# Kernel tuning notes

Measured on AMD Instinct MI355X. Metric: run time of the kernel, lower is better.

## Reference

```python
import jax, jax.numpy as jnp
import numpy as np

HEADS = 8
WSZ = 8
DIM_KEY = 32
DIM_VALUE = 32
DIM = 256
EPS = 1e-5


def setup_inputs() -> dict:
    key = jax.random.key(0)
    ks = jax.random.split(key, 8)
    B, C, H, W = 16, DIM, 128, 128
    inner_k = DIM_KEY * HEADS
    inner_v = DIM_VALUE * HEADS
    x = jax.random.normal(ks[0], (B, C, H, W), dtype=jnp.float32)
    g = jnp.ones((C,), dtype=jnp.float32)
    b = jnp.zeros((C,), dtype=jnp.float32)
    wq = jax.random.normal(ks[1], (inner_k, C), dtype=jnp.float32) * (C ** -0.5)
    wk = jax.random.normal(ks[2], (inner_k, C), dtype=jnp.float32) * (C ** -0.5)
    wv = jax.random.normal(ks[3], (inner_v, C), dtype=jnp.float32) * (C ** -0.5)
    local_w = jax.random.normal(ks[4], (inner_v, inner_v, 3, 3), dtype=jnp.float32) * ((inner_v * 9) ** -0.5)
    local_b = jnp.zeros((inner_v,), dtype=jnp.float32)
    out_w = jax.random.normal(ks[5], (C, inner_v), dtype=jnp.float32) * (inner_v ** -0.5)
    out_b = jnp.zeros((C,), dtype=jnp.float32)
    return {"x": x, "g": g, "b": b, "wq": wq, "wk": wk, "wv": wv,
            "local_w": local_w, "local_b": local_b, "out_w": out_w, "out_b": out_b}


def _to_windows(t, heads, wsz):
    # [B, heads*d, H, W] -> [B*X*Y, heads, wsz*wsz, d]
    B, Ch, H, W = t.shape
    d = Ch // heads
    X, Y = H // wsz, W // wsz
    t = t.reshape(B, heads, d, X, wsz, Y, wsz)
    t = t.transpose(0, 3, 5, 1, 4, 6, 2)  # B X Y heads w1 w2 d
    return t.reshape(B * X * Y, heads, wsz * wsz, d)


def _from_windows(t, B, heads, wsz, H, W):
    X, Y = H // wsz, W // wsz
    d = t.shape[-1]
    t = t.reshape(B, X, Y, heads, wsz, wsz, d)
    t = t.transpose(0, 3, 6, 1, 4, 2, 5)  # B heads d X w1 Y w2
    return t.reshape(B, heads * d, H, W)


def reference(x, g, b, wq, wk, wv, local_w, local_b, out_w, out_b):
    B, C, H, W = x.shape
    # ChanLayerNorm over channel dim (biased var)
    mean = jnp.mean(x, axis=1, keepdims=True)
    var = jnp.var(x, axis=1, keepdims=True)
    xn = (x - mean) / jnp.sqrt(var + EPS) * g[None, :, None, None] + b[None, :, None, None]
    # 1x1 conv projections as einsum
    q = jnp.einsum('oc,bchw->bohw', wq, xn)
    k = jnp.einsum('oc,bchw->bohw', wk, xn)
    v = jnp.einsum('oc,bchw->bohw', wv, xn)
    # local interactive 3x3 conv on v
    local_out = jax.lax.conv_general_dilated(
        v, local_w, window_strides=(1, 1), padding='SAME',
        dimension_numbers=('NCHW', 'OIHW', 'NCHW')) + local_b[None, :, None, None]
    # windowed attention
    qw = _to_windows(q, HEADS, WSZ)
    kw = _to_windows(k, HEADS, WSZ)
    vw = _to_windows(v, HEADS, WSZ)
    scale = DIM_KEY ** -0.5
    dots = jnp.einsum('whid,whjd->whij', qw, kw) * scale
    attn = jax.nn.softmax(dots, axis=-1)
    out = jnp.einsum('whij,whjd->whid', attn, vw)
    out = _from_windows(out, B, HEADS, WSZ, H, W)
    out = out + local_out
    # to_out 1x1 conv with bias
    return jnp.einsum('oc,bchw->bohw', out_w, out) + out_b[None, :, None, None]
```

## Files before the change

### kernel.cpp

```cpp
#include <hip/hip_runtime.h>

typedef __attribute__((ext_vector_type(8))) short short8;
typedef __attribute__((ext_vector_type(4))) float f32x4;
typedef __attribute__((ext_vector_type(2))) _Float16 h2;

#define DEV static __device__ __forceinline__

typedef __attribute__((address_space(1))) void GVoid;
typedef __attribute__((address_space(3))) void LVoid;

DEV unsigned short f2bf(float f) {
  unsigned u = __builtin_bit_cast(unsigned, f);
  u += 0x7fffu + ((u >> 16) & 1u);
  return (unsigned short)(u >> 16);
}
DEV float bf2f(unsigned short h) {
  unsigned u = ((unsigned)h) << 16;
  return __builtin_bit_cast(float, u);
}
DEV void cp16(void* lds_uniform_base, const void* gsrc) {
  __builtin_amdgcn_global_load_lds((GVoid*)gsrc, (LVoid*)lds_uniform_base, 16, 0, 0);
}
DEV float fdot2(h2 a, h2 b, float c) {
  return __builtin_amdgcn_fdot2(a, b, c, false);
}
DEV h2 bch2(float f) { return __builtin_bit_cast(h2, f); }

DEV void xcd_remap(int& mb, int& nb) {
  const int gx = gridDim.x;
  const int p = blockIdx.x + gx * blockIdx.y;
  const int nwg = gx * gridDim.y;
  const int q = nwg >> 3;
  const int L = (p & 7) * q + (p >> 3);
  mb = L % gx;
  nb = L / gx;
}

__global__ __launch_bounds__(256) void setup_kernel(
    const float* __restrict__ wq, const float* __restrict__ wk, const float* __restrict__ wv,
    const float* __restrict__ lw, const float* __restrict__ ow,
    unsigned short* __restrict__ wqkvb, unsigned short* __restrict__ w2b,
    unsigned short* __restrict__ woutb, unsigned short* __restrict__ zp)
{
  int i = blockIdx.x * 256 + threadIdx.x;
  if (i < 196608) {
    float f = (i < 65536) ? wq[i] : (i < 131072) ? wk[i - 65536] : wv[i - 131072];
    wqkvb[i] = f2bf(f);
  } else if (i < 786432) {
    int j = i - 196608;
    int co = j / 2304;
    int r = j - co * 2304;
    int tap = r >> 8;
    int ci = r & 255;
    w2b[j] = f2bf(lw[(co * 256 + ci) * 9 + tap]);
  } else if (i < 851968) {
    int j = i - 786432;
    woutb[j] = f2bf(ow[j]);
  } else if (i < 852096) {
    zp[i - 851968] = 0;
  }
}

__global__ __launch_bounds__(256) void ln_kernel(
    const float* __restrict__ x, const float* __restrict__ gw,
    const float* __restrict__ bw, unsigned short* __restrict__ xn)
{
  const int t = threadIdx.x;
  const int p = blockIdx.x * 256 + t;
  const int b = p >> 14;
  const int pix = p & 16383;
  const int h = pix >> 7;
  const int w = pix & 127;
  const float* xp = x + ((size_t)b << 22) + pix;

  float sum = 0.f, ss = 0.f;
#pragma unroll 8
  for (int c = 0; c < 256; ++c) {
    float f = xp[(size_t)c << 14];
    sum += f;
    ss += f * f;
  }
  float mean = sum * (1.f / 256.f);
  float var = ss * (1.f / 256.f) - mean * mean;
  float inv = rsqrtf(var + 1e-5f);

  const int pw = ((b * 16 + (h >> 3)) * 16 + (w >> 3)) * 64 + (h & 7) * 8 + (w & 7);
  unsigned short* op = xn + (size_t)pw * 256;
#pragma unroll 2
  for (int c = 0; c < 256; c += 4) {
    float f0 = xp[(size_t)(c + 0) << 14];
    float f1 = xp[(size_t)(c + 1) << 14];
    float f2 = xp[(size_t)(c + 2) << 14];
    float f3 = xp[(size_t)(c + 3) << 14];
    float v0 = (f0 - mean) * inv * gw[c + 0] + bw[c + 0];
    float v1 = (f1 - mean) * inv * gw[c + 1] + bw[c + 1];
    float v2 = (f2 - mean) * inv * gw[c + 2] + bw[c + 2];
    float v3 = (f3 - mean) * inv * gw[c + 3] + bw[c + 3];
    unsigned long long pk = (unsigned long long)f2bf(v0) |
                            ((unsigned long long)f2bf(v1) << 16) |
                            ((unsigned long long)f2bf(v2) << 32) |
                            ((unsigned long long)f2bf(v3) << 48);
    *(unsigned long long*)(op + c) = pk;
  }
}

DEV void mfma_tile(const unsigned short* As, const unsigned short* Bs,
                   int wm, int wn, int l15, int quad, f32x4 (&acc)[4][4])
{
  const int sx = l15 & 7;
#pragma unroll
  for (int ks = 0; ks < 2; ++ks) {
    const int sl = ((ks * 4 + quad) ^ sx) * 8;
    short8 a[4], b[4];
#pragma unroll
    for (int i = 0; i < 4; ++i)
      a[i] = *(const short8*)(As + (wm + i * 16 + l15) * 64 + sl);
#pragma unroll
    for (int j = 0; j < 4; ++j)
      b[j] = *(const short8*)(Bs + (wn + j * 16 + l15) * 64 + sl);
#pragma unroll
    for (int i = 0; i < 4; ++i)
#pragma unroll
      for (int j = 0; j < 4; ++j)
        acc[i][j] = __builtin_amdgcn_mfma_f32_16x16x32_bf16(a[i], b[j], acc[i][j], 0, 0, 0);
  }
}

__global__ __launch_bounds__(256) void qkv_gemm(
    const unsigned short* __restrict__ wqkvb, const unsigned short* __restrict__ xn,
    unsigned short* __restrict__ qb, unsigned short* __restrict__ kb,
    unsigned short* __restrict__ vb)
{
  __shared__ __align__(16) unsigned short As[128 * 64];
  __shared__ __align__(16) unsigned short Bs[128 * 64];
  const int tid = threadIdx.x;
  const int lane = tid & 63;
  const int wave = tid >> 6;
  const int l15 = lane & 15;
  const int quad = lane >> 4;
  const int wm = (wave >> 1) * 64;
  const int wn = (wave & 1) * 64;
  const int sub = tid & 7;
  const int row0 = tid >> 3;
  const int ssub = sub ^ (row0 & 7);
  int mb, nb;
  xcd_remap(mb, nb);
  const int m0 = mb * 128;
  const int n0 = nb * 128;

  f32x4 acc[4][4];
  f32x4 zero = {0.f, 0.f, 0.f, 0.f};
#pragma unroll
  for (int i = 0; i < 4; ++i)
#pragma unroll
    for (int j = 0; j < 4; ++j) acc[i][j] = zero;

  for (int kt = 0; kt < 4; ++kt) {
    const int k0 = kt * 64;
#pragma unroll
    for (int it = 0; it < 4; ++it) {
      const int row = it * 32 + row0;
      cp16(As + (size_t)(it * 256 + wave * 64) * 8,
           wqkvb + (size_t)(m0 + row) * 256 + k0 + ssub * 8);
      cp16(Bs + (size_t)(it * 256 + wave * 64) * 8,
           xn + (size_t)(n0 + row) * 256 + k0 + ssub * 8);
    }
    __syncthreads();
    mfma_tile(As, Bs, wm, wn, l15, quad, acc);
    __syncthreads();
  }

  unsigned short* ob = (m0 < 256) ? qb : (m0 < 512) ? kb : vb;
  const int chb = (m0 & 255) + wm;
#pragma unroll
  for (int i = 0; i < 4; ++i) {
    const int ch = chb + i * 16 + quad * 4;
#pragma unroll
    for (int j = 0; j < 4; ++j) {
      const int n = n0 + wn + j * 16 + l15;
      unsigned long long pk = (unsigned long long)f2bf(acc[i][j][0]) |
                              ((unsigned long long)f2bf(acc[i][j][1]) << 16) |
                              ((unsigned long long)f2bf(acc[i][j][2]) << 32) |
                              ((unsigned long long)f2bf(acc[i][j][3]) << 48);
      *(unsigned long long*)(ob + (size_t)n * 256 + ch) = pk;
    }
  }
}

__global__ __launch_bounds__(128) void attn_kernel(
    const unsigned short* __restrict__ qb, const unsigned short* __restrict__ kb,
    const unsigned short* __restrict__ vb, unsigned short* __restrict__ attnb)
{
  __shared__ __align__(16) _Float16 ks2[2][64][40];
  __shared__ __align__(16) _Float16 vs2[2][32][64];
  const int tid = threadIdx.x;
  const int tok = tid & 63;
  const int hs = tid >> 6;
  const int win = blockIdx.x >> 2;
  const int head = (blockIdx.x & 3) * 2 + hs;
  const size_t base = (size_t)(win * 64 + tok) * 256 + head * 32;

  h2 q2[16];
  {
    const uint4* qp4 = (const uint4*)(qb + base);
    const uint4* kp4 = (const uint4*)(kb + base);
    const uint4* vp4 = (const uint4*)(vb + base);
#pragma unroll
    for (int i = 0; i < 4; ++i) {
      uint4 u = qp4[i];
      unsigned uu[4] = {u.x, u.y, u.z, u.w};
#pragma unroll
      for (int w = 0; w < 4; ++w) {
        h2 p;
        p.x = (_Float16)bf2f((unsigned short)(uu[w] & 0xffff));
        p.y = (_Float16)bf2f((unsigned short)(uu[w] >> 16));
        q2[i * 4 + w] = p;
      }
    }
#pragma unroll
    for (int i = 0; i < 4; ++i) {
      uint4 u = kp4[i];
      unsigned uu[4] = {u.x, u.y, u.z, u.w};
#pragma unroll
      for (int w = 0; w < 4; ++w) {
        int c = 2 * (i * 4 + w);
        ks2[hs][tok][c + 0] = (_Float16)bf2f((unsigned short)(uu[w] & 0xffff));
        ks2[hs][tok][c + 1] = (_Float16)bf2f((unsigned short)(uu[w] >> 16));
      }
      uint4 v = vp4[i];
      unsigned vv[4] = {v.x, v.y, v.z, v.w};
#pragma unroll
      for (int w = 0; w < 4; ++w) {
        int c = 2 * (i * 4 + w);
        vs2[hs][c + 0][tok] = (_Float16)bf2f((unsigned short)(vv[w] & 0xffff));
        vs2[hs][c + 1][tok] = (_Float16)bf2f((unsigned short)(vv[w] >> 16));
      }
    }
  }
  __syncthreads();

  float dots[64];
#pragma unroll 4
  for (int j = 0; j < 64; ++j) {
    const float4* kr = (const float4*)ks2[hs][j];
    float d = 0.f;
#pragma unroll
    for (int qq = 0; qq < 4; ++qq) {
      float4 raw = kr[qq];
      d = fdot2(q2[4 * qq + 0], bch2(raw.x), d);
      d = fdot2(q2[4 * qq + 1], bch2(raw.y), d);
      d = fdot2(q2[4 * qq + 2], bch2(raw.z), d);
      d = fdot2(q2[4 * qq + 3], bch2(raw.w), d);
    }
    dots[j] = d * 0.17677669529663688f;
  }
  float mx = -1e30f;
#pragma unroll
  for (int j = 0; j < 64; ++j) mx = fmaxf(mx, dots[j]);
  float s = 0.f;
#pragma unroll
  for (int j = 0; j < 64; ++j) {
    float e = __expf(dots[j] - mx);
    dots[j] = e;
    s += e;
  }
  const float rs = 1.f / s;

  h2 p2[32];
#pragma unroll
  for (int jp = 0; jp < 32; ++jp) {
    h2 p;
    p.x = (_Float16)dots[2 * jp];
    p.y = (_Float16)dots[2 * jp + 1];
    p2[jp] = p;
  }

  float of[32];
#pragma unroll 4
  for (int c = 0; c < 32; ++c) {
    const float4* vr = (const float4*)vs2[hs][c];
    float o = 0.f;
#pragma unroll
    for (int qq = 0; qq < 8; ++qq) {
      float4 raw = vr[qq];
      o = fdot2(p2[4 * qq + 0], bch2(raw.x), o);
      o = fdot2(p2[4 * qq + 1], bch2(raw.y), o);
      o = fdot2(p2[4 * qq + 2], bch2(raw.z), o);
      o = fdot2(p2[4 * qq + 3], bch2(raw.w), o);
    }
    of[c] = o;
  }

  uint4* op4 = (uint4*)(attnb + base);
#pragma unroll
  for (int i = 0; i < 4; ++i) {
    uint4 o;
    o.x = (unsigned)f2bf(of[8 * i + 0] * rs) | ((unsigned)f2bf(of[8 * i + 1] * rs) << 16);
    o.y = (unsigned)f2bf(of[8 * i + 2] * rs) | ((unsigned)f2bf(of[8 * i + 3] * rs) << 16);
    o.z = (unsigned)f2bf(of[8 * i + 4] * rs) | ((unsigned)f2bf(of[8 * i + 5] * rs) << 16);
    o.w = (unsigned)f2bf(of[8 * i + 6] * rs) | ((unsigned)f2bf(of[8 * i + 7] * rs) << 16);
    op4[i] = o;
  }
}

__global__ __launch_bounds__(256) void conv_gemm(
    const unsigned short* __restrict__ w2b, const unsigned short* __restrict__ vbuf,
    const unsigned short* __restrict__ attnb, const float* __restrict__ lbias,
    const unsigned short* __restrict__ zp, unsigned short* __restrict__ sumb)
{
  __shared__ __align__(16) unsigned short As[128 * 64];
  __shared__ __align__(16) unsigned short Bs[128 * 64];
  const int tid = threadIdx.x;
  const int lane = tid & 63;
  const int wave = tid >> 6;
  const int l15 = lane & 15;
  const int quad = lane >> 4;
  const int wm = (wave >> 1) * 64;
  const int wn = (wave & 1) * 64;
  const int sub = tid & 7;
  const int row0 = tid >> 3;
  const int ssub = sub ^ (row0 & 7);
  int mb, nb;
  xcd_remap(mb, nb);
  const int m0 = mb * 128;
  const int n0 = nb * 128;

  int bi[4], hh[4], ww[4];
#pragma unroll
  for (int it = 0; it < 4; ++it) {
    int n = n0 + it * 32 + row0;
    int b = n >> 14;
    int r = n & 16383;
    int Xw = r >> 10;
    int r2 = r & 1023;
    int Yw = r2 >> 6;
    int t2 = r2 & 63;
    bi[it] = b;
    hh[it] = Xw * 8 + (t2 >> 3);
    ww[it] = Yw * 8 + (t2 & 7);
  }

  f32x4 acc[4][4];
  f32x4 zero = {0.f, 0.f, 0.f, 0.f};
#pragma unroll
  for (int i = 0; i < 4; ++i)
#pragma unroll
    for (int j = 0; j < 4; ++j) acc[i][j] = zero;

  for (int tap = 0; tap < 9; ++tap) {
    const int dy = tap / 3 - 1;
    const int dx = tap - (tap / 3) * 3 - 1;
    const unsigned short* bp[4];
    int bstep[4];
#pragma unroll
    for (int it = 0; it < 4; ++it) {
      int h2_ = hh[it] + dy, w2_ = ww[it] + dx;
      bool ok = ((unsigned)h2_ < 128u) && ((unsigned)w2_ < 128u);
      int nn = ((bi[it] * 16 + (h2_ >> 3)) * 16 + (w2_ >> 3)) * 64 + (h2_ & 7) * 8 + (w2_ & 7);
      bp[it] = ok ? (vbuf + (size_t)nn * 256 + ssub * 8) : (zp + ssub * 8);
      bstep[it] = ok ? 64 : 0;
    }
    for (int cc = 0; cc < 4; ++cc) {
#pragma unroll
      for (int it = 0; it < 4; ++it) {
        cp16(As + (size_t)(it * 256 + wave * 64) * 8,
             w2b + ((size_t)(m0 + it * 32 + row0) * 9 + tap) * 256 + cc * 64 + ssub * 8);
        cp16(Bs + (size_t)(it * 256 + wave * 64) * 8, bp[it] + cc * bstep[it]);
      }
      __syncthreads();
      mfma_tile(As, Bs, wm, wn, l15, quad, acc);
      __syncthreads();
    }
  }

#pragma unroll
  for (int i = 0; i < 4; ++i) {
    const int ch = m0 + wm + i * 16 + quad * 4;
    const float b0 = lbias[ch + 0], b1 = lbias[ch + 1], b2 = lbias[ch + 2], b3 = lbias[ch + 3];
#pragma unroll
    for (int j = 0; j < 4; ++j) {
      const int n = n0 + wn + j * 16 + l15;
      const unsigned* ap = (const unsigned*)(attnb + (size_t)n * 256 + ch);
      unsigned a0 = ap[0], a1 = ap[1];
      float r0 = acc[i][j][0] + b0 + bf2f((unsigned short)(a0 & 0xffff));
      float r1 = acc[i][j][1] + b1 + bf2f((unsigned short)(a0 >> 16));
      float r2 = acc[i][j][2] + b2 + bf2f((unsigned short)(a1 & 0xffff));
      float r3 = acc[i][j][3] + b3 + bf2f((unsigned short)(a1 >> 16));
      unsigned long long pk = (unsigned long long)f2bf(r0) |
                              ((unsigned long long)f2bf(r1) << 16) |
                              ((unsigned long long)f2bf(r2) << 32) |
                              ((unsigned long long)f2bf(r3) << 48);
      *(unsigned long long*)(sumb + (size_t)n * 256 + ch) = pk;
    }
  }
}

__global__ __launch_bounds__(256) void out_gemm(
    const unsigned short* __restrict__ woutb, const unsigned short* __restrict__ sumb,
    const float* __restrict__ obias, float* __restrict__ out)
{
  __shared__ __align__(16) unsigned short As[128 * 64];
  __shared__ __align__(16) unsigned short Bs[128 * 64];
  const int tid = threadIdx.x;
  const int lane = tid & 63;
  const int wave = tid >> 6;
  const int l15 = lane & 15;
  const int quad = lane >> 4;
  const int wm = (wave >> 1) * 64;
  const int wn = (wave & 1) * 64;
  const int sub = tid & 7;
  const int row0 = tid >> 3;
  const int ssub = sub ^ (row0 & 7);
  int mb, nb;
  xcd_remap(mb, nb);
  const int m0 = mb * 128;
  const int n0 = nb * 128;

  f32x4 acc[4][4];
  f32x4 zero = {0.f, 0.f, 0.f, 0.f};
#pragma unroll
  for (int i = 0; i < 4; ++i)
#pragma unroll
    for (int j = 0; j < 4; ++j) acc[i][j] = zero;

  for (int kt = 0; kt < 4; ++kt) {
    const int k0 = kt * 64;
#pragma unroll
    for (int it = 0; it < 4; ++it) {
      const int row = it * 32 + row0;
      cp16(As + (size_t)(it * 256 + wave * 64) * 8,
           woutb + (size_t)(m0 + row) * 256 + k0 + ssub * 8);
      cp16(Bs + (size_t)(it * 256 + wave * 64) * 8,
           sumb + (size_t)(n0 + row) * 256 + k0 + ssub * 8);
    }
    __syncthreads();
    mfma_tile(As, Bs, wm, wn, l15, quad, acc);
    __syncthreads();
  }

  int bb4[4], hw4[4];
#pragma unroll
  for (int j = 0; j < 4; ++j) {
    int n = n0 + wn + j * 16 + l15;
    int b = n >> 14;
    int r = n & 16383;
    int Xw = r >> 10;
    int r2 = r & 1023;
    int Yw = r2 >> 6;
    int t2 = r2 & 63;
    bb4[j] = b;
    hw4[j] = (Xw * 8 + (t2 >> 3)) * 128 + Yw * 8 + (t2 & 7);
  }
#pragma unroll
  for (int i = 0; i < 4; ++i) {
    const int mb2 = m0 + wm + i * 16 + quad * 4;
    const float o0 = obias[mb2 + 0], o1 = obias[mb2 + 1], o2 = obias[mb2 + 2], o3 = obias[mb2 + 3];
#pragma unroll
    for (int j = 0; j < 4; ++j) {
      float* o = out + ((size_t)(bb4[j] * 256 + mb2) << 14) + hw4[j];
      o[0] = acc[i][j][0] + o0;
      o[(size_t)1 << 14] = acc[i][j][1] + o1;
      o[(size_t)2 << 14] = acc[i][j][2] + o2;
      o[(size_t)3 << 14] = acc[i][j][3] + o3;
    }
  }
}

extern "C" void kernel_launch(void* const* d_in, const int* in_sizes, int n_in,
                              void* d_out, int out_size, void* d_ws, size_t ws_size,
                              hipStream_t stream)
{
  const float* x  = (const float*)d_in[0];
  const float* g  = (const float*)d_in[1];
  const float* bb = (const float*)d_in[2];
  const float* wq = (const float*)d_in[3];
  const float* wk = (const float*)d_in[4];
  const float* wv = (const float*)d_in[5];
  const float* lw = (const float*)d_in[6];
  const float* lb = (const float*)d_in[7];
  const float* ow = (const float*)d_in[8];
  const float* ob = (const float*)d_in[9];
  float* out = (float*)d_out;

  char* ws = (char*)d_ws;
  unsigned short* wqkvb = (unsigned short*)(ws + 0);
  unsigned short* w2b   = (unsigned short*)(ws + 393216);
  unsigned short* woutb = (unsigned short*)(ws + 1572864);
  unsigned short* zp    = (unsigned short*)(ws + 1703936);
  const size_t BUF0 = 1704192;

  int nimg = 16;
  while (nimg > 1 && BUF0 + 4ull * (size_t)nimg * 8388608ull > ws_size) nimg >>= 1;
  const size_t bufB = (size_t)nimg * 8388608ull;
  unsigned short* xnb = (unsigned short*)(ws + BUF0);
  unsigned short* qb  = (unsigned short*)(ws + BUF0 + bufB);
  unsigned short* kb  = (unsigned short*)(ws + BUF0 + 2 * bufB);
  unsigned short* vb  = (unsigned short*)(ws + BUF0 + 3 * bufB);
  unsigned short* attnb = xnb;
  unsigned short* sumb  = qb;

  setup_kernel<<<3329, 256, 0, stream>>>(wq, wk, wv, lw, ow, wqkvb, w2b, woutb, zp);

  const int nchunk = 16 / nimg;
  const int Nc = nimg * 16384;
  for (int c = 0; c < nchunk; ++c) {
    const float* xc = x + (size_t)c * nimg * 256 * 16384;
    float* oc = out + (size_t)c * nimg * 256 * 16384;
    ln_kernel<<<Nc / 256, 256, 0, stream>>>(xc, g, bb, xnb);
    qkv_gemm<<<dim3(6, Nc / 128), 256, 0, stream>>>(wqkvb, xnb, qb, kb, vb);
    attn_kernel<<<(Nc / 64) * 4, 128, 0, stream>>>(qb, kb, vb, attnb);
    conv_gemm<<<dim3(2, Nc / 128), 256, 0, stream>>>(w2b, vb, attnb, lb, zp, sumb);
    out_gemm<<<dim3(2, Nc / 128), 256, 0, stream>>>(woutb, sumb, ob, oc);
  }
}
```

Before: 1.751 ms.

## Switch intermediate storage and MFMA from bf16 to fp16 throughout pipeline

```diff
diff --git a/kernel.cpp b/kernel.cpp
--- a/kernel.cpp
+++ b/kernel.cpp
@@ -3,20 +3,25 @@
 typedef __attribute__((ext_vector_type(8))) short short8;
 typedef __attribute__((ext_vector_type(4))) float f32x4;
 typedef __attribute__((ext_vector_type(2))) _Float16 h2;
+typedef __attribute__((ext_vector_type(8))) _Float16 h8;
 
 #define DEV static __device__ __forceinline__
 
 typedef __attribute__((address_space(1))) void GVoid;
 typedef __attribute__((address_space(3))) void LVoid;
 
-DEV unsigned short f2bf(float f) {
-  unsigned u = __builtin_bit_cast(unsigned, f);
-  u += 0x7fffu + ((u >> 16) & 1u);
-  return (unsigned short)(u >> 16);
-}
-DEV float bf2f(unsigned short h) {
-  unsigned u = ((unsigned)h) << 16;
-  return __builtin_bit_cast(float, u);
+DEV unsigned short f2h(float f) {
+  _Float16 h = (_Float16)f;
+  return __builtin_bit_cast(unsigned short, h);
+}
+DEV float h2f(unsigned short u) {
+  return (float)__builtin_bit_cast(_Float16, u);
+}
+DEV unsigned pkh(float a, float b) {
+  h2 h;
+  h.x = (_Float16)a;
+  h.y = (_Float16)b;
+  return __builtin_bit_cast(unsigned, h);
 }
 DEV void cp16(void* lds_uniform_base, const void* gsrc) {
   __builtin_amdgcn_global_load_lds((GVoid*)gsrc, (LVoid*)lds_uniform_base, 16, 0, 0);
@@ -24,7 +29,6 @@
 DEV float fdot2(h2 a, h2 b, float c) {
   return __builtin_amdgcn_fdot2(a, b, c, false);
 }
-DEV h2 bch2(float f) { return __builtin_bit_cast(h2, f); }
 
 DEV void xcd_remap(int& mb, int& nb) {
   const int gx = gridDim.x;
@@ -45,17 +49,17 @@
   int i = blockIdx.x * 256 + threadIdx.x;
   if (i < 196608) {
     float f = (i < 65536) ? wq[i] : (i < 131072) ? wk[i - 65536] : wv[i - 131072];
-    wqkvb[i] = f2bf(f);
+    wqkvb[i] = f2h(f);
   } else if (i < 786432) {
     int j = i - 196608;
     int co = j / 2304;
     int r = j - co * 2304;
     int tap = r >> 8;
     int ci = r & 255;
-    w2b[j] = f2bf(lw[(co * 256 + ci) * 9 + tap]);
+    w2b[j] = f2h(lw[(co * 256 + ci) * 9 + tap]);
   } else if (i < 851968) {
     int j = i - 786432;
-    woutb[j] = f2bf(ow[j]);
+    woutb[j] = f2h(ow[j]);
   } else if (i < 852096) {
     zp[i - 851968] = 0;
   }
@@ -96,10 +100,8 @@
     float v1 = (f1 - mean) * inv * gw[c + 1] + bw[c + 1];
     float v2 = (f2 - mean) * inv * gw[c + 2] + bw[c + 2];
     float v3 = (f3 - mean) * inv * gw[c + 3] + bw[c + 3];
-    unsigned long long pk = (unsigned long long)f2bf(v0) |
-                            ((unsigned long long)f2bf(v1) << 16) |
-                            ((unsigned long long)f2bf(v2) << 32) |
-                            ((unsigned long long)f2bf(v3) << 48);
+    unsigned long long pk = (unsigned long long)pkh(v0, v1) |
+                            ((unsigned long long)pkh(v2, v3) << 32);
     *(unsigned long long*)(op + c) = pk;
   }
 }
@@ -122,7 +124,8 @@
     for (int i = 0; i < 4; ++i)
 #pragma unroll
       for (int j = 0; j < 4; ++j)
-        acc[i][j] = __builtin_amdgcn_mfma_f32_16x16x32_bf16(a[i], b[j], acc[i][j], 0, 0, 0);
+        acc[i][j] = __builtin_amdgcn_mfma_f32_16x16x32_f16(
+            __builtin_bit_cast(h8, a[i]), __builtin_bit_cast(h8, b[j]), acc[i][j], 0, 0, 0);
   }
 }
 
@@ -178,10 +181,8 @@
 #pragma unroll
     for (int j = 0; j < 4; ++j) {
       const int n = n0 + wn + j * 16 + l15;
-      unsigned long long pk = (unsigned long long)f2bf(acc[i][j][0]) |
-                              ((unsigned long long)f2bf(acc[i][j][1]) << 16) |
-                              ((unsigned long long)f2bf(acc[i][j][2]) << 32) |
-                              ((unsigned long long)f2bf(acc[i][j][3]) << 48);
+      unsigned long long pk = (unsigned long long)pkh(acc[i][j][0], acc[i][j][1]) |
+                              ((unsigned long long)pkh(acc[i][j][2], acc[i][j][3]) << 32);
       *(unsigned long long*)(ob + (size_t)n * 256 + ch) = pk;
     }
   }
@@ -205,54 +206,45 @@
     const uint4* qp4 = (const uint4*)(qb + base);
     const uint4* kp4 = (const uint4*)(kb + base);
     const uint4* vp4 = (const uint4*)(vb + base);
+    const _Float16 sc = (_Float16)0.17677669529663688f;
+    h2 sc2;
+    sc2.x = sc;
+    sc2.y = sc;
 #pragma unroll
     for (int i = 0; i < 4; ++i) {
       uint4 u = qp4[i];
-      unsigned uu[4] = {u.x, u.y, u.z, u.w};
-#pragma unroll
-      for (int w = 0; w < 4; ++w) {
-        h2 p;
-        p.x = (_Float16)bf2f((unsigned short)(uu[w] & 0xffff));
-        p.y = (_Float16)bf2f((unsigned short)(uu[w] >> 16));
-        q2[i * 4 + w] = p;
-      }
-    }
-#pragma unroll
-    for (int i = 0; i < 4; ++i) {
-      uint4 u = kp4[i];
-      unsigned uu[4] = {u.x, u.y, u.z, u.w};
-#pragma unroll
-      for (int w = 0; w < 4; ++w) {
-        int c = 2 * (i * 4 + w);
-        ks2[hs][tok][c + 0] = (_Float16)bf2f((unsigned short)(uu[w] & 0xffff));
-        ks2[hs][tok][c + 1] = (_Float16)bf2f((unsigned short)(uu[w] >> 16));
-      }
+      q2[i * 4 + 0] = __builtin_bit_cast(h2, u.x) * sc2;
+      q2[i * 4 + 1] = __builtin_bit_cast(h2, u.y) * sc2;
+      q2[i * 4 + 2] = __builtin_bit_cast(h2, u.z) * sc2;
+      q2[i * 4 + 3] = __builtin_bit_cast(h2, u.w) * sc2;
+      *(uint4*)&ks2[hs][tok][8 * i] = kp4[i];
       uint4 v = vp4[i];
       unsigned vv[4] = {v.x, v.y, v.z, v.w};
 #pragma unroll
       for (int w = 0; w < 4; ++w) {
+        h2 hv = __builtin_bit_cast(h2, vv[w]);
         int c = 2 * (i * 4 + w);
-        vs2[hs][c + 0][tok] = (_Float16)bf2f((unsigned short)(vv[w] & 0xffff));
-        vs2[hs][c + 1][tok] = (_Float16)bf2f((unsigned short)(vv[w] >> 16));
+        vs2[hs][c + 0][tok] = hv.x;
+        vs2[hs][c + 1][tok] = hv.y;
       }
     }
   }
   __syncthreads();
 
   float dots[64];
-#pragma unroll 4
+#pragma unroll
   for (int j = 0; j < 64; ++j) {
-    const float4* kr = (const float4*)ks2[hs][j];
+    const uint4* kr = (const uint4*)ks2[hs][j];
     float d = 0.f;
 #pragma unroll
     for (int qq = 0; qq < 4; ++qq) {
-      float4 raw = kr[qq];
-      d = fdot2(q2[4 * qq + 0], bch2(raw.x), d);
-      d = fdot2(q2[4 * qq + 1], bch2(raw.y), d);
-      d = fdot2(q2[4 * qq + 2], bch2(raw.z), d);
-      d = fdot2(q2[4 * qq + 3], bch2(raw.w), d);
-    }
-    dots[j] = d * 0.17677669529663688f;
+      uint4 raw = kr[qq];
+      d = fdot2(q2[4 * qq + 0], __builtin_bit_cast(h2, raw.x), d);
+      d = fdot2(q2[4 * qq + 1], __builtin_bit_cast(h2, raw.y), d);
+      d = fdot2(q2[4 * qq + 2], __builtin_bit_cast(h2, raw.z), d);
+      d = fdot2(q2[4 * qq + 3], __builtin_bit_cast(h2, raw.w), d);
+    }
+    dots[j] = d;
   }
   float mx = -1e30f;
 #pragma unroll
@@ -276,17 +268,17 @@
   }
 
   float of[32];
-#pragma unroll 4
+#pragma unroll
   for (int c = 0; c < 32; ++c) {
-    const float4* vr = (const float4*)vs2[hs][c];
+    const uint4* vr = (const uint4*)vs2[hs][c];
     float o = 0.f;
 #pragma unroll
     for (int qq = 0; qq < 8; ++qq) {
-      float4 raw = vr[qq];
-      o = fdot2(p2[4 * qq + 0], bch2(raw.x), o);
-      o = fdot2(p2[4 * qq + 1], bch2(raw.y), o);
-      o = fdot2(p2[4 * qq + 2], bch2(raw.z), o);
-      o = fdot2(p2[4 * qq + 3], bch2(raw.w), o);
+      uint4 raw = vr[qq];
+      o = fdot2(p2[4 * qq + 0], __builtin_bit_cast(h2, raw.x), o);
+      o = fdot2(p2[4 * qq + 1], __builtin_bit_cast(h2, raw.y), o);
+      o = fdot2(p2[4 * qq + 2], __builtin_bit_cast(h2, raw.z), o);
+      o = fdot2(p2[4 * qq + 3], __builtin_bit_cast(h2, raw.w), o);
     }
     of[c] = o;
   }
@@ -295,10 +287,10 @@
 #pragma unroll
   for (int i = 0; i < 4; ++i) {
     uint4 o;
-    o.x = (unsigned)f2bf(of[8 * i + 0] * rs) | ((unsigned)f2bf(of[8 * i + 1] * rs) << 16);
-    o.y = (unsigned)f2bf(of[8 * i + 2] * rs) | ((unsigned)f2bf(of[8 * i + 3] * rs) << 16);
-    o.z = (unsigned)f2bf(of[8 * i + 4] * rs) | ((unsigned)f2bf(of[8 * i + 5] * rs) << 16);
-    o.w = (unsigned)f2bf(of[8 * i + 6] * rs) | ((unsigned)f2bf(of[8 * i + 7] * rs) << 16);
+    o.x = pkh(of[8 * i + 0] * rs, of[8 * i + 1] * rs);
+    o.y = pkh(of[8 * i + 2] * rs, of[8 * i + 3] * rs);
+    o.z = pkh(of[8 * i + 4] * rs, of[8 * i + 5] * rs);
+    o.w = pkh(of[8 * i + 6] * rs, of[8 * i + 7] * rs);
     op4[i] = o;
   }
 }
@@ -382,14 +374,12 @@
       const int n = n0 + wn + j * 16 + l15;
       const unsigned* ap = (const unsigned*)(attnb + (size_t)n * 256 + ch);
       unsigned a0 = ap[0], a1 = ap[1];
-      float r0 = acc[i][j][0] + b0 + bf2f((unsigned short)(a0 & 0xffff));
-      float r1 = acc[i][j][1] + b1 + bf2f((unsigned short)(a0 >> 16));
-      float r2 = acc[i][j][2] + b2 + bf2f((unsigned short)(a1 & 0xffff));
-      float r3 = acc[i][j][3] + b3 + bf2f((unsigned short)(a1 >> 16));
-      unsigned long long pk = (unsigned long long)f2bf(r0) |
-                              ((unsigned long long)f2bf(r1) << 16) |
-                              ((unsigned long long)f2bf(r2) << 32) |
-                              ((unsigned long long)f2bf(r3) << 48);
+      float r0 = acc[i][j][0] + b0 + h2f((unsigned short)(a0 & 0xffff));
+      float r1 = acc[i][j][1] + b1 + h2f((unsigned short)(a0 >> 16));
+      float r2 = acc[i][j][2] + b2 + h2f((unsigned short)(a1 & 0xffff));
+      float r3 = acc[i][j][3] + b3 + h2f((unsigned short)(a1 >> 16));
+      unsigned long long pk = (unsigned long long)pkh(r0, r1) |
+                              ((unsigned long long)pkh(r2, r3) << 32);
       *(unsigned long long*)(sumb + (size_t)n * 256 + ch) = pk;
     }
   }
```

After: 1.497 ms. 1.17x faster.
